# Kernel tuning notes

Hardware: AMD Instinct MI355X
Metric: run time of the kernel (lower is better)

The kernel has to match this reference:

```python
import jax, jax.numpy as jnp
import numpy as np

N = 4096      # particles
E = 262144    # interacting pairs (~64 neighbors each)
H = 128       # MLP hidden width
FD = 6        # force/velocity DOF (force + torque)
FEAT = 7      # rel(3) + dist + r_sq + r_quad + min_dist
IN_DIM = FEAT + 2 * FD  # 19


def setup_inputs() -> dict:
    key = jax.random.key(0)
    ks = jax.random.split(key, 10)
    rel_vecs = jax.random.normal(ks[0], (N, N, 3), jnp.float32)
    target_indices = jax.random.randint(ks[1], (E,), 0, N, dtype=jnp.int64)
    source_indices = jax.random.randint(ks[2], (E,), 0, N, dtype=jnp.int64)
    force = jax.random.normal(ks[3], (N, FD), jnp.float32)
    viscosity = jnp.ones((1,), jnp.float32)
    s1 = 1.0 / np.sqrt(IN_DIM)
    s2 = 1.0 / np.sqrt(H)
    W1 = jax.random.normal(ks[4], (IN_DIM, H), jnp.float32) * s1
    b1 = jnp.zeros((H,), jnp.float32)
    W2 = jax.random.normal(ks[5], (H, H), jnp.float32) * s2
    b2 = jnp.zeros((H,), jnp.float32)
    W3 = jax.random.normal(ks[6], (H, FD), jnp.float32) * s2
    b3 = jnp.zeros((FD,), jnp.float32)
    median = jnp.float32(2.5)
    contact_distance = jnp.float32(2.0)
    return {
        'rel_vecs': rel_vecs, 'target_indices': target_indices,
        'source_indices': source_indices, 'force': force,
        'viscosity': viscosity, 'median': median,
        'contact_distance': contact_distance,
        'W1': W1, 'b1': b1, 'W2': W2, 'b2': b2, 'W3': W3, 'b3': b3,
    }


def _predict_velocity(features, f_t, f_s, mu, W1, b1, W2, b2, W3, b3):
    # MLP over concatenated pair features + both forces; Stokes flow is
    # linear in force/viscosity, so scale output by 1/mu.
    x = jnp.concatenate([features, f_t, f_s], axis=-1)  # [E, 19]
    h = jax.nn.relu(x @ W1 + b1)
    h = jax.nn.relu(h @ W2 + b2)
    return (h @ W3 + b3) / mu  # [E, FD]


def reference(rel_vecs, target_indices, source_indices, force, viscosity,
              median, contact_distance, W1, b1, W2, b2, W3, b3):
    # Gather pairwise relative vectors: [E, 3]
    rel_selected = rel_vecs[target_indices, source_indices]
    dist = jnp.maximum(
        jnp.linalg.norm(rel_selected, axis=-1, keepdims=True), 1e-8)  # [E,1]
    r_shift = dist - median
    r_sq = r_shift * r_shift
    r_quad = r_sq * r_sq
    min_dist = dist - contact_distance
    features = jnp.concatenate(
        [rel_selected, dist, r_sq, r_quad, min_dist], axis=-1)  # [E, 7]
    force_target = force[target_indices]  # [E, FD]
    force_source = force[source_indices]  # [E, FD]
    mu = jnp.asarray(viscosity, dtype=force.dtype).reshape(())
    vel = _predict_velocity(features, force_target, force_source, mu,
                            W1, b1, W2, b2, W3, b3)  # [E, FD]
    # Scatter-add per-target contributions
    contribution = jnp.zeros_like(force).at[target_indices].add(vel)
    return contribution
```

## Files before the change

### kernel.cpp

```cpp
#include <hip/hip_runtime.h>

#define NPART 4096
#define E_TOT 262144
#define HID   128
#define FDOF  6
#define BM    64
#define NIT   (E_TOT / BM)
#define GRID  1024
#define XPAD  40
#define HPAD  136
#define NCOPY 8
#define OUTSZ (NPART * FDOF)

typedef __bf16 bf16x8 __attribute__((ext_vector_type(8)));
typedef float  f32x4  __attribute__((ext_vector_type(4)));

__global__ void pairvel_zero_kernel(float* __restrict__ p, int n) {
    const int i = blockIdx.x * blockDim.x + threadIdx.x;
    if (i < n) p[i] = 0.0f;
}

__global__ void pairvel_reduce_kernel(const float* __restrict__ wsp,
                                      float* __restrict__ out) {
    const int i = blockIdx.x * blockDim.x + threadIdx.x;
    if (i < OUTSZ) {
        float s = 0.0f;
        #pragma unroll
        for (int c = 0; c < NCOPY; ++c) s += wsp[c * OUTSZ + i];
        out[i] = s;
    }
}

__global__ __launch_bounds__(256) void pairvel_mfma_kernel(
    const float* __restrict__ rel,
    const int*   __restrict__ tgt,
    const int*   __restrict__ src,
    const float* __restrict__ force,
    const float* __restrict__ visc,
    const float* __restrict__ medianp,
    const float* __restrict__ contactp,
    const float* __restrict__ W1,
    const float* __restrict__ b1,
    const float* __restrict__ W2,
    const float* __restrict__ b2,
    const float* __restrict__ W3,
    const float* __restrict__ b3,
    float* __restrict__ wsp)
{
    const int tid = threadIdx.x;
    const int w   = tid >> 6;
    const int l   = tid & 63;
    const int l15 = l & 15;
    const int lhi = l >> 4;

    float* __restrict__ outc = wsp + (size_t)(blockIdx.x & (NCOPY - 1)) * OUTSZ;

    bf16x8 w1f[2], w2f[4][2], w3f[4];
    #pragma unroll
    for (int nb = 0; nb < 2; ++nb) {
        const int n = (2 * w + nb) * 16 + l15;
        #pragma unroll
        for (int r = 0; r < 8; ++r) {
            const int k = lhi * 8 + r;
            w1f[nb][r] = (k < 19) ? (__bf16)W1[k * HID + n] : (__bf16)0.0f;
        }
    }
    #pragma unroll
    for (int kt = 0; kt < 4; ++kt)
        #pragma unroll
        for (int nb = 0; nb < 2; ++nb) {
            const int n = (2 * w + nb) * 16 + l15;
            #pragma unroll
            for (int r = 0; r < 8; ++r)
                w2f[kt][nb][r] = (__bf16)W2[(kt * 32 + lhi * 8 + r) * HID + n];
        }
    #pragma unroll
    for (int kt = 0; kt < 4; ++kt)
        #pragma unroll
        for (int r = 0; r < 8; ++r) {
            const int k = kt * 32 + lhi * 8 + r;
            w3f[kt][r] = (l15 < FDOF) ? (__bf16)W3[k * FDOF + l15] : (__bf16)0.0f;
        }

    const float b1v0 = b1[(2 * w) * 16 + l15];
    const float b1v1 = b1[(2 * w + 1) * 16 + l15];
    const float b2v0 = b2[(2 * w) * 16 + l15];
    const float b2v1 = b2[(2 * w + 1) * 16 + l15];
    const float b3v  = (l15 < FDOF) ? b3[l15] : 0.0f;
    const float inv_mu  = 1.0f / visc[0];
    const float median  = medianp[0];
    const float contact = contactp[0];

    __shared__ __align__(16) __bf16 Xs[2][BM][XPAD];
    __shared__ __align__(16) __bf16 Hs[BM][HPAD];
    __shared__ int tgts[2][BM];

    for (int t = tid; t < 2 * BM * 13; t += 256) {
        const int b = t / (BM * 13), rem = t % (BM * 13);
        Xs[b][rem / 13][19 + rem % 13] = (__bf16)0.0f;
    }

    int   p_i0 = 0;
    float p_v0 = 0.f, p_v1 = 0.f, p_v2 = 0.f;
    float p_f3 = 0.f, p_f4 = 0.f, p_f5 = 0.f;

    auto gather_load = [&](int e0n) {
        if (tid < BM) {
            const int eg = e0n + tid;
            p_i0 = tgt[eg];
            const int sg = src[eg];
            const float* rp = rel + ((size_t)p_i0 * NPART + sg) * 3;
            p_v0 = rp[0]; p_v1 = rp[1]; p_v2 = rp[2];
        } else if (tid < 2 * BM) {
            const int eg = e0n + (tid - BM);
            const float2* f2 =
                reinterpret_cast<const float2*>(force + (size_t)tgt[eg] * FDOF);
            const float2 u0 = f2[0], u1 = f2[1], u2 = f2[2];
            p_v0 = u0.x; p_v1 = u0.y; p_v2 = u1.x;
            p_f3 = u1.y; p_f4 = u2.x; p_f5 = u2.y;
        } else if (tid < 3 * BM) {
            const int eg = e0n + (tid - 2 * BM);
            const float2* f2 =
                reinterpret_cast<const float2*>(force + (size_t)src[eg] * FDOF);
            const float2 u0 = f2[0], u1 = f2[1], u2 = f2[2];
            p_v0 = u0.x; p_v1 = u0.y; p_v2 = u1.x;
            p_f3 = u1.y; p_f4 = u2.x; p_f5 = u2.y;
        }
    };

    auto write_x = [&](int b) {
        if (tid < BM) {
            const int e = tid;
            tgts[b][e] = p_i0;
            const float dist = fmaxf(
                sqrtf(p_v0 * p_v0 + p_v1 * p_v1 + p_v2 * p_v2), 1e-8f);
            const float rs = (dist - median) * (dist - median);
            Xs[b][e][0] = (__bf16)p_v0;
            Xs[b][e][1] = (__bf16)p_v1;
            Xs[b][e][2] = (__bf16)p_v2;
            Xs[b][e][3] = (__bf16)dist;
            Xs[b][e][4] = (__bf16)rs;
            Xs[b][e][5] = (__bf16)(rs * rs);
            Xs[b][e][6] = (__bf16)(dist - contact);
        } else if (tid < 2 * BM) {
            const int e = tid - BM;
            Xs[b][e][7]  = (__bf16)p_v0;
            Xs[b][e][8]  = (__bf16)p_v1;
            Xs[b][e][9]  = (__bf16)p_v2;
            Xs[b][e][10] = (__bf16)p_f3;
            Xs[b][e][11] = (__bf16)p_f4;
            Xs[b][e][12] = (__bf16)p_f5;
        } else if (tid < 3 * BM) {
            const int e = tid - 2 * BM;
            Xs[b][e][13] = (__bf16)p_v0;
            Xs[b][e][14] = (__bf16)p_v1;
            Xs[b][e][15] = (__bf16)p_v2;
            Xs[b][e][16] = (__bf16)p_f3;
            Xs[b][e][17] = (__bf16)p_f4;
            Xs[b][e][18] = (__bf16)p_f5;
        }
    };

    gather_load(blockIdx.x * BM);
    write_x(0);
    if (blockIdx.x + GRID < NIT) gather_load((blockIdx.x + GRID) * BM);
    int buf = 0;

    for (int it = blockIdx.x; it < NIT; it += GRID) {
        __syncthreads();

        #pragma unroll
        for (int m = 0; m < 4; ++m) {
            const bf16x8 a = *reinterpret_cast<const bf16x8*>(
                &Xs[buf][m * 16 + l15][lhi * 8]);
            #pragma unroll
            for (int nb = 0; nb < 2; ++nb) {
                const float bv = nb ? b1v1 : b1v0;
                f32x4 acc = { bv, bv, bv, bv };
                acc = __builtin_amdgcn_mfma_f32_16x16x32_bf16(
                          a, w1f[nb], acc, 0, 0, 0);
                #pragma unroll
                for (int r = 0; r < 4; ++r)
                    Hs[m * 16 + lhi * 4 + r][(2 * w + nb) * 16 + l15] =
                        (__bf16)fmaxf(acc[r], 0.0f);
            }
        }
        __syncthreads();

        f32x4 accs[4][2];
        #pragma unroll
        for (int m = 0; m < 4; ++m) {
            accs[m][0] = (f32x4){ b2v0, b2v0, b2v0, b2v0 };
            accs[m][1] = (f32x4){ b2v1, b2v1, b2v1, b2v1 };
            #pragma unroll
            for (int kt = 0; kt < 4; ++kt) {
                const bf16x8 a = *reinterpret_cast<const bf16x8*>(
                    &Hs[m * 16 + l15][kt * 32 + lhi * 8]);
                accs[m][0] = __builtin_amdgcn_mfma_f32_16x16x32_bf16(
                                 a, w2f[kt][0], accs[m][0], 0, 0, 0);
                accs[m][1] = __builtin_amdgcn_mfma_f32_16x16x32_bf16(
                                 a, w2f[kt][1], accs[m][1], 0, 0, 0);
            }
        }
        __syncthreads();

        #pragma unroll
        for (int m = 0; m < 4; ++m)
            #pragma unroll
            for (int nb = 0; nb < 2; ++nb)
                #pragma unroll
                for (int r = 0; r < 4; ++r)
                    Hs[m * 16 + lhi * 4 + r][(2 * w + nb) * 16 + l15] =
                        (__bf16)fmaxf(accs[m][nb][r], 0.0f);

        if (it + GRID < NIT) write_x(buf ^ 1);
        if (it + 2 * GRID < NIT)
            gather_load((it + 2 * GRID) * BM);
        __syncthreads();

        f32x4 acc3 = { 0.0f, 0.0f, 0.0f, 0.0f };
        #pragma unroll
        for (int kt = 0; kt < 4; ++kt) {
            const bf16x8 a = *reinterpret_cast<const bf16x8*>(
                &Hs[w * 16 + l15][kt * 32 + lhi * 8]);
            acc3 = __builtin_amdgcn_mfma_f32_16x16x32_bf16(
                       a, w3f[kt], acc3, 0, 0, 0);
        }
        if (l15 < FDOF) {
            #pragma unroll
            for (int r = 0; r < 4; ++r) {
                const int e = w * 16 + lhi * 4 + r;
                atomicAdd(&outc[(size_t)tgts[buf][e] * FDOF + l15],
                          (acc3[r] + b3v) * inv_mu);
            }
        }
        buf ^= 1;
    }
}

extern "C" void kernel_launch(void* const* d_in, const int* in_sizes, int n_in,
                              void* d_out, int out_size, void* d_ws, size_t ws_size,
                              hipStream_t stream) {
    const float* rel   = (const float*)d_in[0];
    const int*   tgt   = (const int*)d_in[1];
    const int*   src   = (const int*)d_in[2];
    const float* force = (const float*)d_in[3];
    const float* visc  = (const float*)d_in[4];
    const float* med   = (const float*)d_in[5];
    const float* con   = (const float*)d_in[6];
    const float* W1    = (const float*)d_in[7];
    const float* b1    = (const float*)d_in[8];
    const float* W2    = (const float*)d_in[9];
    const float* b2    = (const float*)d_in[10];
    const float* W3    = (const float*)d_in[11];
    const float* b3    = (const float*)d_in[12];
    float* out = (float*)d_out;
    float* wsp = (float*)d_ws;

    const int nws = NCOPY * OUTSZ;
    pairvel_zero_kernel<<<(nws + 255) / 256, 256, 0, stream>>>(wsp, nws);
    pairvel_mfma_kernel<<<GRID, 256, 0, stream>>>(
        rel, tgt, src, force, visc, med, con, W1, b1, W2, b2, W3, b3, wsp);
    pairvel_reduce_kernel<<<(OUTSZ + 255) / 256, 256, 0, stream>>>(wsp, out);
}
```

Baseline: 50.73 us.

## Double grid to two tiles per block, move W3 to LDS, single X buffer

Grid size goes from 1024 to 2048 blocks so each block handles exactly two 64-edge tiles, and the loop is fully unrolled. Indices for both tiles are loaded up front, and the second tile's gathers are issued between layer 1 and layer 2 of the first tile. W3 fragments now live in LDS instead of registers, and X uses a single buffer, which lowers register and LDS pressure to raise occupancy. The cost is extra LDS reads for W3 and the weight-fragment setup being repeated across twice as many blocks.

```diff
diff --git a/kernel.cpp b/kernel.cpp
--- a/kernel.cpp
+++ b/kernel.cpp
@@ -6,7 +6,7 @@
 #define FDOF  6
 #define BM    64
 #define NIT   (E_TOT / BM)
-#define GRID  1024
+#define GRID  2048
 #define XPAD  40
 #define HPAD  136
 #define NCOPY 8
@@ -47,15 +47,16 @@
     const float* __restrict__ b3,
     float* __restrict__ wsp)
 {
-    const int tid = threadIdx.x;
-    const int w   = tid >> 6;
-    const int l   = tid & 63;
-    const int l15 = l & 15;
-    const int lhi = l >> 4;
+    const int tid  = threadIdx.x;
+    const int w    = tid >> 6;
+    const int l    = tid & 63;
+    const int l15  = l & 15;
+    const int lhi  = l >> 4;
+    const int mye  = l;
 
     float* __restrict__ outc = wsp + (size_t)(blockIdx.x & (NCOPY - 1)) * OUTSZ;
 
-    bf16x8 w1f[2], w2f[4][2], w3f[4];
+    bf16x8 w1f[2], w2f[4][2];
     #pragma unroll
     for (int nb = 0; nb < 2; ++nb) {
         const int n = (2 * w + nb) * 16 + l15;
@@ -73,13 +74,6 @@
             #pragma unroll
             for (int r = 0; r < 8; ++r)
                 w2f[kt][nb][r] = (__bf16)W2[(kt * 32 + lhi * 8 + r) * HID + n];
-        }
-    #pragma unroll
-    for (int kt = 0; kt < 4; ++kt)
-        #pragma unroll
-        for (int r = 0; r < 8; ++r) {
-            const int k = kt * 32 + lhi * 8 + r;
-            w3f[kt][r] = (l15 < FDOF) ? (__bf16)W3[k * FDOF + l15] : (__bf16)0.0f;
         }
 
     const float b1v0 = b1[(2 * w) * 16 + l15];
@@ -91,88 +85,91 @@
     const float median  = medianp[0];
     const float contact = contactp[0];
 
-    __shared__ __align__(16) __bf16 Xs[2][BM][XPAD];
+    __shared__ __align__(16) __bf16 Xs[BM][XPAD];
     __shared__ __align__(16) __bf16 Hs[BM][HPAD];
+    __shared__ __align__(16) __bf16 W3L[4][64][8];
     __shared__ int tgts[2][BM];
 
-    for (int t = tid; t < 2 * BM * 13; t += 256) {
-        const int b = t / (BM * 13), rem = t % (BM * 13);
-        Xs[b][rem / 13][19 + rem % 13] = (__bf16)0.0f;
-    }
-
-    int   p_i0 = 0;
-    float p_v0 = 0.f, p_v1 = 0.f, p_v2 = 0.f;
-    float p_f3 = 0.f, p_f4 = 0.f, p_f5 = 0.f;
-
-    auto gather_load = [&](int e0n) {
-        if (tid < BM) {
-            const int eg = e0n + tid;
-            p_i0 = tgt[eg];
-            const int sg = src[eg];
-            const float* rp = rel + ((size_t)p_i0 * NPART + sg) * 3;
-            p_v0 = rp[0]; p_v1 = rp[1]; p_v2 = rp[2];
-        } else if (tid < 2 * BM) {
-            const int eg = e0n + (tid - BM);
-            const float2* f2 =
-                reinterpret_cast<const float2*>(force + (size_t)tgt[eg] * FDOF);
+    {
+        const int kt = tid >> 6, ln = tid & 63;
+        const int c  = ln & 15, rh = ln >> 4;
+        bf16x8 v;
+        #pragma unroll
+        for (int r = 0; r < 8; ++r)
+            v[r] = (c < FDOF) ? (__bf16)W3[(kt * 32 + rh * 8 + r) * FDOF + c]
+                              : (__bf16)0.0f;
+        *reinterpret_cast<bf16x8*>(&W3L[kt][ln][0]) = v;
+    }
+
+    for (int t = tid; t < BM * 13; t += 256)
+        Xs[t / 13][19 + t % 13] = (__bf16)0.0f;
+
+    int tgA = 0, sgA = 0, tgB = 0, sgB = 0;
+    if (w < 3) {
+        const int eA = blockIdx.x * BM + mye;
+        const int eB = (blockIdx.x + GRID) * BM + mye;
+        tgA = tgt[eA]; sgA = src[eA];
+        tgB = tgt[eB]; sgB = src[eB];
+    }
+
+    float p0 = 0.f, p1 = 0.f, p2 = 0.f, p3 = 0.f, p4 = 0.f, p5 = 0.f;
+
+    auto gather_data = [&](int tg, int sg) {
+        if (w == 0) {
+            const float* rp = rel + ((size_t)tg * NPART + sg) * 3;
+            p0 = rp[0]; p1 = rp[1]; p2 = rp[2];
+        } else if (w == 1) {
+            const float2* f2 = (const float2*)(force + (size_t)tg * FDOF);
             const float2 u0 = f2[0], u1 = f2[1], u2 = f2[2];
-            p_v0 = u0.x; p_v1 = u0.y; p_v2 = u1.x;
-            p_f3 = u1.y; p_f4 = u2.x; p_f5 = u2.y;
-        } else if (tid < 3 * BM) {
-            const int eg = e0n + (tid - 2 * BM);
-            const float2* f2 =
-                reinterpret_cast<const float2*>(force + (size_t)src[eg] * FDOF);
+            p0 = u0.x; p1 = u0.y; p2 = u1.x; p3 = u1.y; p4 = u2.x; p5 = u2.y;
+        } else if (w == 2) {
+            const float2* f2 = (const float2*)(force + (size_t)sg * FDOF);
             const float2 u0 = f2[0], u1 = f2[1], u2 = f2[2];
-            p_v0 = u0.x; p_v1 = u0.y; p_v2 = u1.x;
-            p_f3 = u1.y; p_f4 = u2.x; p_f5 = u2.y;
+            p0 = u0.x; p1 = u0.y; p2 = u1.x; p3 = u1.y; p4 = u2.x; p5 = u2.y;
         }
     };
 
-    auto write_x = [&](int b) {
-        if (tid < BM) {
-            const int e = tid;
-            tgts[b][e] = p_i0;
-            const float dist = fmaxf(
-                sqrtf(p_v0 * p_v0 + p_v1 * p_v1 + p_v2 * p_v2), 1e-8f);
+    auto write_x = [&](int b, int tg) {
+        if (w == 0) {
+            tgts[b][mye] = tg;
+            const float dist = fmaxf(sqrtf(p0*p0 + p1*p1 + p2*p2), 1e-8f);
             const float rs = (dist - median) * (dist - median);
-            Xs[b][e][0] = (__bf16)p_v0;
-            Xs[b][e][1] = (__bf16)p_v1;
-            Xs[b][e][2] = (__bf16)p_v2;
-            Xs[b][e][3] = (__bf16)dist;
-            Xs[b][e][4] = (__bf16)rs;
-            Xs[b][e][5] = (__bf16)(rs * rs);
-            Xs[b][e][6] = (__bf16)(dist - contact);
-        } else if (tid < 2 * BM) {
-            const int e = tid - BM;
-            Xs[b][e][7]  = (__bf16)p_v0;
-            Xs[b][e][8]  = (__bf16)p_v1;
-            Xs[b][e][9]  = (__bf16)p_v2;
-            Xs[b][e][10] = (__bf16)p_f3;
-            Xs[b][e][11] = (__bf16)p_f4;
-            Xs[b][e][12] = (__bf16)p_f5;
-        } else if (tid < 3 * BM) {
-            const int e = tid - 2 * BM;
-            Xs[b][e][13] = (__bf16)p_v0;
-            Xs[b][e][14] = (__bf16)p_v1;
-            Xs[b][e][15] = (__bf16)p_v2;
-            Xs[b][e][16] = (__bf16)p_f3;
-            Xs[b][e][17] = (__bf16)p_f4;
-            Xs[b][e][18] = (__bf16)p_f5;
+            Xs[mye][0] = (__bf16)p0;
+            Xs[mye][1] = (__bf16)p1;
+            Xs[mye][2] = (__bf16)p2;
+            Xs[mye][3] = (__bf16)dist;
+            Xs[mye][4] = (__bf16)rs;
+            Xs[mye][5] = (__bf16)(rs * rs);
+            Xs[mye][6] = (__bf16)(dist - contact);
+        } else if (w == 1) {
+            Xs[mye][7]  = (__bf16)p0;
+            Xs[mye][8]  = (__bf16)p1;
+            Xs[mye][9]  = (__bf16)p2;
+            Xs[mye][10] = (__bf16)p3;
+            Xs[mye][11] = (__bf16)p4;
+            Xs[mye][12] = (__bf16)p5;
+        } else if (w == 2) {
+            Xs[mye][13] = (__bf16)p0;
+            Xs[mye][14] = (__bf16)p1;
+            Xs[mye][15] = (__bf16)p2;
+            Xs[mye][16] = (__bf16)p3;
+            Xs[mye][17] = (__bf16)p4;
+            Xs[mye][18] = (__bf16)p5;
         }
     };
 
-    gather_load(blockIdx.x * BM);
-    write_x(0);
-    if (blockIdx.x + GRID < NIT) gather_load((blockIdx.x + GRID) * BM);
+    gather_data(tgA, sgA);
+    write_x(0, tgA);
     int buf = 0;
 
-    for (int it = blockIdx.x; it < NIT; it += GRID) {
+    #pragma unroll
+    for (int ii = 0; ii < 2; ++ii) {
         __syncthreads();
 
         #pragma unroll
         for (int m = 0; m < 4; ++m) {
             const bf16x8 a = *reinterpret_cast<const bf16x8*>(
-                &Xs[buf][m * 16 + l15][lhi * 8]);
+                &Xs[m * 16 + l15][lhi * 8]);
             #pragma unroll
             for (int nb = 0; nb < 2; ++nb) {
                 const float bv = nb ? b1v1 : b1v0;
@@ -187,6 +184,8 @@
         }
         __syncthreads();
 
+        if (ii == 0) gather_data(tgB, sgB);
+
         f32x4 accs[4][2];
         #pragma unroll
         for (int m = 0; m < 4; ++m) {
@@ -213,9 +212,7 @@
                     Hs[m * 16 + lhi * 4 + r][(2 * w + nb) * 16 + l15] =
                         (__bf16)fmaxf(accs[m][nb][r], 0.0f);
 
-        if (it + GRID < NIT) write_x(buf ^ 1);
-        if (it + 2 * GRID < NIT)
-            gather_load((it + 2 * GRID) * BM);
+        if (ii == 0) write_x(buf ^ 1, tgB);
         __syncthreads();
 
         f32x4 acc3 = { 0.0f, 0.0f, 0.0f, 0.0f };
@@ -223,8 +220,10 @@
         for (int kt = 0; kt < 4; ++kt) {
             const bf16x8 a = *reinterpret_cast<const bf16x8*>(
                 &Hs[w * 16 + l15][kt * 32 + lhi * 8]);
+            const bf16x8 wf = *reinterpret_cast<const bf16x8*>(
+                &W3L[kt][l][0]);
             acc3 = __builtin_amdgcn_mfma_f32_16x16x32_bf16(
-                       a, w3f[kt], acc3, 0, 0, 0);
+                       a, wf, acc3, 0, 0, 0);
         }
         if (l15 < FDOF) {
             #pragma unroll
```

Measured after the change: 52.60 us. +3.7%, slower.
